# Optimization experiments

Hardware: AMD Instinct MI355X
Metric: run time of the kernel (lower is better)

## Reference

```python
import jax, jax.numpy as jnp
import numpy as np

N = 200_000   # nodes
E = 4_000_000 # edges
R = 4         # edge types
D = 64        # hidden_dim
V = 256       # opcode vocab
G = 64        # graphs in batch
C = 10        # classes


def setup_inputs() -> dict:
    key = jax.random.key(0)
    ks = jax.random.split(key, 24)
    inp = {
        "x_op": jax.random.randint(ks[0], (N,), 0, V, dtype=jnp.int32),
        "x_cat": jax.random.randint(ks[1], (N,), 0, 3, dtype=jnp.int32),
        "edge_index": jax.random.randint(ks[2], (2, E), 0, N, dtype=jnp.int32),
        "edge_type": jax.random.randint(ks[3], (E,), 0, R, dtype=jnp.int32),
        "batch": jnp.sort(jax.random.randint(ks[4], (N,), 0, G, dtype=jnp.int32)),
        "op_emb": jax.random.normal(ks[5], (V, D), jnp.float32) * 0.02,
        "cat_emb": jax.random.normal(ks[6], (3, D), jnp.float32) * 0.02,
    }
    for i in range(1, 4):
        inp[f"w{i}"] = jax.random.normal(ks[6 + 3 * i], (R, D, D), jnp.float32) * 0.02
        inp[f"r{i}"] = jax.random.normal(ks[7 + 3 * i], (D, D), jnp.float32) * 0.02
        inp[f"b{i}"] = jnp.zeros((D,), jnp.float32)
    inp["fc1_w"] = jax.random.normal(ks[20], (D, D), jnp.float32) * 0.02
    inp["fc1_b"] = jnp.zeros((D,), jnp.float32)
    inp["fc2_w"] = jax.random.normal(ks[21], (D, C), jnp.float32) * 0.02
    inp["fc2_b"] = jnp.zeros((C,), jnp.float32)
    return inp


def rgcn_layer(h, src, tgt, etype, w, root, bias):
    # PyG RGCNConv semantics: per-relation linear transform, per-relation
    # MEAN aggregation over incoming edges, summed over relations,
    # plus root transform and bias.
    n, d = h.shape
    r = w.shape[0]
    trans = jnp.einsum('nd,rde->rne', h, w)        # [R, N, d]
    msg = trans[etype, src]                         # [E, d] gather
    seg = tgt.astype(jnp.int32) * r + etype         # combined (node, relation) key
    s = jax.ops.segment_sum(msg, seg, num_segments=n * r)
    cnt = jax.ops.segment_sum(jnp.ones((msg.shape[0],), h.dtype), seg, num_segments=n * r)
    agg = (s / jnp.maximum(cnt, 1.0)[:, None]).reshape(n, r, d).sum(axis=1)
    return agg + h @ root + bias


def reference(x_op, x_cat, edge_index, edge_type, batch,
              op_emb, cat_emb,
              w1, r1, b1, w2, r2, b2, w3, r3, b3,
              fc1_w, fc1_b, fc2_w, fc2_b):
    src, tgt = edge_index[0], edge_index[1]
    h = op_emb[x_op] + cat_emb[x_cat]               # [N, D]
    h = jax.nn.relu(rgcn_layer(h, src, tgt, edge_type, w1, r1, b1))
    # dropout p=0.2 is identity in eval mode
    h = jax.nn.relu(rgcn_layer(h, src, tgt, edge_type, w2, r2, b2))
    h = rgcn_layer(h, src, tgt, edge_type, w3, r3, b3)
    # global mean pool over graphs
    sums = jax.ops.segment_sum(h, batch, num_segments=G)
    cnts = jax.ops.segment_sum(jnp.ones((h.shape[0],), h.dtype), batch, num_segments=G)
    pooled = sums / jnp.maximum(cnts, 1.0)[:, None]  # [G, D]
    h = jax.nn.relu(pooled @ fc1_w + fc1_b)
    out = h @ fc2_w + fc2_b
    return jax.nn.log_softmax(out, axis=1)
```

## Files before the change

### kernel.cpp

```cpp
#include <hip/hip_runtime.h>
#include <hip/hip_bf16.h>

#define N_NODES 200000
#define N_EDGES 4000000
#define R_REL   4
#define D_DIM   64
#define G_GRAPHS 64
#define C_CLS   10
#define NR      (N_NODES * R_REL)
#define POOL_BLOCKS 128

#define NCB   391
#define LCAP  64
#define CCAP  11264
#define EPB   8192

#define EMBED_BLOCKS 12500
#define BOUNDS_BLOCKS 782

#define MS    72

typedef __attribute__((ext_vector_type(8))) short short8v;
typedef __attribute__((ext_vector_type(4))) float f32x4;

__device__ __forceinline__ unsigned short to_bf16(float x) {
    __hip_bfloat16 b = __float2bfloat16(x);
    return *(unsigned short*)&b;
}

#define ACC8(u) \
    a0 += __uint_as_float((u).x << 16); \
    a1 += __uint_as_float((u).x & 0xFFFF0000u); \
    a2 += __uint_as_float((u).y << 16); \
    a3 += __uint_as_float((u).y & 0xFFFF0000u); \
    a4 += __uint_as_float((u).z << 16); \
    a5 += __uint_as_float((u).z & 0xFFFF0000u); \
    a6 += __uint_as_float((u).w << 16); \
    a7 += __uint_as_float((u).w & 0xFFFF0000u);


__global__ __launch_bounds__(512) void k_coarse(
    const int* __restrict__ src, const int* __restrict__ tgt,
    const int* __restrict__ et,
    int* __restrict__ gcur, unsigned int* __restrict__ coarse) {
    __shared__ unsigned int bins[NCB * LCAP];
    __shared__ int lcnt[NCB], lpos[NCB];

    const int tid = threadIdx.x;
    for (int i = tid; i < NCB; i += 512) lcnt[i] = 0;
    __syncthreads();

#pragma unroll
    for (int h = 0; h < 4; ++h) {
        int e4 = blockIdx.x * EPB + (h * 512 + tid) * 4;
        if (e4 < N_EDGES) {
            int4 s = *(const int4*)&src[e4];
            int4 t = *(const int4*)&tgt[e4];
            int4 r = *(const int4*)&et[e4];
#define PUT(ss, tt, rr) { \
                int key = (tt) * R_REL + (rr); \
                int b = key >> 11; \
                int p = atomicAdd(&lcnt[b], 1); \
                if (p < LCAP) bins[b * LCAP + p] = \
                    ((unsigned int)(key & 2047) << 18) | (unsigned int)(ss); \
            }
            PUT(s.x, t.x, r.x); PUT(s.y, t.y, r.y);
            PUT(s.z, t.z, r.z); PUT(s.w, t.w, r.w);
#undef PUT
        }
    }
    __syncthreads();

    for (int i = tid; i < NCB; i += 512) {
        int c = lcnt[i]; if (c > LCAP) c = LCAP;
        lcnt[i] = c;
        lpos[i] = atomicAdd(&gcur[i], c);
    }
    __syncthreads();

    for (int j = tid; j < NCB * LCAP; j += 512) {
        int b = j >> 6, l = j & 63;
        if (l < lcnt[b]) {
            int gp = lpos[b] + l;
            if (gp < CCAP) coarse[(size_t)b * CCAP + gp] = bins[j];
        }
    }
}


__global__ __launch_bounds__(1024) void k_fine(
    const int* __restrict__ gcur, const unsigned int* __restrict__ coarse,
    int* __restrict__ off, int* __restrict__ srcSorted) {
    __shared__ unsigned int ent[CCAP];
    __shared__ int hist[2048];
    __shared__ int pre[512];

    const int cb = blockIdx.x, tid = threadIdx.x;

    int v = 0;
    if (tid < 512) {
        v = (tid < NCB) ? gcur[tid] : 0;
        if (v > CCAP) v = CCAP;
        pre[tid] = v;
    }
    __syncthreads();
    for (int d = 1; d < 512; d <<= 1) {
        int t = 0;
        if (tid < 512 && tid >= d) t = pre[tid - d];
        __syncthreads();
        if (tid < 512) pre[tid] += t;
        __syncthreads();
    }
    const int gb = (cb > 0) ? pre[cb - 1] : 0;

    int cnt = gcur[cb]; if (cnt > CCAP) cnt = CCAP;
    const int key0 = cb << 11;
    const unsigned int* cp = coarse + (size_t)cb * CCAP;

    for (int i = tid; i < cnt; i += 1024) ent[i] = cp[i];
    hist[tid] = 0; hist[tid + 1024] = 0;
    __syncthreads();

    for (int i = tid; i < cnt; i += 1024) atomicAdd(&hist[ent[i] >> 18], 1);
    __syncthreads();

    int x0 = hist[tid], x1 = hist[tid + 1024];
    for (int d = 1; d < 2048; d <<= 1) {
        int v0 = (tid >= d) ? hist[tid - d] : 0;
        int v1 = hist[tid + 1024 - d];
        __syncthreads();
        hist[tid] += v0;
        hist[tid + 1024] += v1;
        __syncthreads();
    }
    int excl0 = hist[tid] - x0;
    int excl1 = hist[tid + 1024] - x1;
    __syncthreads();
    hist[tid] = excl0;
    hist[tid + 1024] = excl1;

    int key = key0 + tid;
    if (key < NR) off[key] = gb + excl0;
    key = key0 + tid + 1024;
    if (key < NR) off[key] = gb + excl1;
    if (cb == NCB - 1 && tid == 0) off[NR] = N_EDGES;
    __syncthreads();

    for (int i = tid; i < cnt; i += 1024) {
        unsigned int e = ent[i];
        int pos = atomicAdd(&hist[e >> 18], 1);
        srcSorted[gb + pos] = (int)(e & 0x3FFFFu);
    }
}


struct WPtrs { const float* p[15]; };

__global__ void k_misc(const int* __restrict__ xop, const int* __restrict__ xcat,
                       const float4* __restrict__ opemb, const float4* __restrict__ catemb,
                       ushort4* __restrict__ hb,
                       const int* __restrict__ batch, int* __restrict__ start,
                       WPtrs wp, unsigned short* __restrict__ wfrag) {
    int bid = blockIdx.x;
    if (bid < EMBED_BLOCKS) {
        int i = bid * 256 + threadIdx.x;
        if (i < N_NODES * 16) {
            int n = i >> 4, q = i & 15;
            float4 a = opemb[xop[n] * 16 + q];
            float4 b = catemb[xcat[n] * 16 + q];
            ushort4 ub;
            ub.x = to_bf16(a.x + b.x); ub.y = to_bf16(a.y + b.y);
            ub.z = to_bf16(a.z + b.z); ub.w = to_bf16(a.w + b.w);
            hb[i] = ub;
        }
    } else if (bid < EMBED_BLOCKS + BOUNDS_BLOCKS) {
        int i = (bid - EMBED_BLOCKS) * 256 + threadIdx.x;
        if (i >= N_NODES) return;
        int b = batch[i];
        if (i == 0) {
            for (int g = 0; g <= b; ++g) start[g] = 0;
        } else {
            int p = batch[i - 1];
            for (int g = p + 1; g <= b; ++g) start[g] = i;
        }
        if (i == N_NODES - 1) {
            for (int g = b + 1; g <= G_GRAPHS; ++g) start[g] = N_NODES;
        }
    } else {
        int m = bid - EMBED_BLOCKS - BOUNDS_BLOCKS;
        const float* W = wp.p[m];
        unsigned short* outp = wfrag + m * 4096;
        for (int f = threadIdx.x; f < 4096; f += 256) {
            int j = f & 7, lane = (f >> 3) & 63, c0t = (f >> 9) & 3, kk = f >> 11;
            int k  = kk * 32 + (lane >> 4) * 8 + j;
            int ch = c0t * 16 + (lane & 15);
            outp[f] = to_bf16(W[k * 64 + ch]);
        }
    }
}


template <int RELU>
__global__ __launch_bounds__(1024, 2) void k_layer(
    const unsigned short* __restrict__ hb_in,
    unsigned short* __restrict__ hb_out,
    const int* __restrict__ off, const int* __restrict__ srcSorted,
    const unsigned short* __restrict__ wfrag,
    const float* __restrict__ bias)
{
    __shared__ unsigned short m_lds[256 * MS];
    __shared__ unsigned short wf[5 * 4096];

    const int tid  = threadIdx.x;
    const int lane = tid & 63, wid = tid >> 6;
    const int g = lane >> 3, q = lane & 7;
    const int nbase = blockIdx.x * 64;

    for (int i = tid; i < 2560; i += 1024)
        ((uint4*)wf)[i] = ((const uint4*)wfrag)[i];

    const unsigned short* base = hb_in + q * 8;
#pragma unroll
    for (int p = 0; p < 2; ++p) {
        const int keyLocal = wid * 16 + p * 8 + g;
        const int key = nbase * R_REL + keyLocal;
        const int e0 = off[key];
        const int e1 = off[key + 1];

        float a0 = 0.f, a1 = 0.f, a2 = 0.f, a3 = 0.f,
              a4 = 0.f, a5 = 0.f, a6 = 0.f, a7 = 0.f;

        int e = e0;
        for (; e + 4 <= e1; e += 4) {
            int s0 = srcSorted[e];
            int s1 = srcSorted[e + 1];
            int s2 = srcSorted[e + 2];
            int s3 = srcSorted[e + 3];
            uint4 u0 = *(const uint4*)(base + (size_t)s0 * D_DIM);
            uint4 u1 = *(const uint4*)(base + (size_t)s1 * D_DIM);
            uint4 u2 = *(const uint4*)(base + (size_t)s2 * D_DIM);
            uint4 u3 = *(const uint4*)(base + (size_t)s3 * D_DIM);
            ACC8(u0); ACC8(u1); ACC8(u2); ACC8(u3);
        }
        for (; e < e1; ++e) {
            int s0 = srcSorted[e];
            uint4 u0 = *(const uint4*)(base + (size_t)s0 * D_DIM);
            ACC8(u0);
        }

        int deg = e1 - e0;
        const float iv = 1.0f / (float)(deg > 0 ? deg : 1);
        uint4 o;
        o.x = (unsigned int)to_bf16(a0 * iv) | ((unsigned int)to_bf16(a1 * iv) << 16);
        o.y = (unsigned int)to_bf16(a2 * iv) | ((unsigned int)to_bf16(a3 * iv) << 16);
        o.z = (unsigned int)to_bf16(a4 * iv) | ((unsigned int)to_bf16(a5 * iv) << 16);
        o.w = (unsigned int)to_bf16(a6 * iv) | ((unsigned int)to_bf16(a7 * iv) << 16);
        *(uint4*)(&m_lds[keyLocal * MS + q * 8]) = o;
    }
    __syncthreads();

    const int n0 = (wid >> 2) * 16;
    const int ct = wid & 3;
    const int arowL = n0 + (lane & 15);
    const int koff = (lane >> 4) * 8;

    f32x4 acc = {0.f, 0.f, 0.f, 0.f};

#pragma unroll
    for (int r = 0; r < 5; ++r) {
        uint4 a0u, a1u;
        if (r < 4) {
            const unsigned short* ap = &m_lds[(arowL * R_REL + r) * MS];
            a0u = *(const uint4*)(ap + koff);
            a1u = *(const uint4*)(ap + 32 + koff);
        } else {
            const unsigned short* ap = hb_in + (size_t)(nbase + arowL) * D_DIM;
            a0u = *(const uint4*)(ap + koff);
            a1u = *(const uint4*)(ap + 32 + koff);
        }
        const unsigned short* bbase = wf + r * 4096 + ct * 512 + lane * 8;
        uint4 b0u = *(const uint4*)bbase;
        uint4 b1u = *(const uint4*)(bbase + 2048);
        acc = __builtin_amdgcn_mfma_f32_16x16x32_bf16(
            __builtin_bit_cast(short8v, a0u), __builtin_bit_cast(short8v, b0u), acc, 0, 0, 0);
        acc = __builtin_amdgcn_mfma_f32_16x16x32_bf16(
            __builtin_bit_cast(short8v, a1u), __builtin_bit_cast(short8v, b1u), acc, 0, 0, 0);
    }

    float bv = bias[ct * 16 + (lane & 15)];
#pragma unroll
    for (int i = 0; i < 4; ++i) {
        float v = acc[i] + bv;
        if (RELU) v = fmaxf(v, 0.f);
        int n = nbase + n0 + (lane >> 4) * 4 + i;
        hb_out[(size_t)n * D_DIM + ct * 16 + (lane & 15)] = to_bf16(v);
    }
}


__global__ __launch_bounds__(1024) void k_pool(const unsigned short* __restrict__ hb,
                                               const int* __restrict__ batch,
                                               float* __restrict__ partial) {
    __shared__ float bin[G_GRAPHS * D_DIM];
    int tid = threadIdx.x, lane = tid & 63, wid = tid >> 6;
    for (int i = tid; i < G_GRAPHS * D_DIM; i += 1024) bin[i] = 0.f;
    __syncthreads();
    const int per = (N_NODES + POOL_BLOCKS - 1) / POOL_BLOCKS;
    int n0 = blockIdx.x * per;
    int n1 = n0 + per; if (n1 > N_NODES) n1 = N_NODES;
    int cntw = n1 - n0;
    int sub = (cntw + 15) >> 4;
    int w0 = n0 + wid * sub;
    int w1 = w0 + sub; if (w1 > n1) w1 = n1;

    float acc = 0.f;
    int cur = -1;
    for (int n = w0; n < w1; ++n) {
        int b = __builtin_amdgcn_readfirstlane(batch[n]);
        unsigned int u = hb[(size_t)n * D_DIM + lane];
        float v = __uint_as_float(u << 16);
        if (b != cur) {
            if (cur >= 0) atomicAdd(&bin[cur * D_DIM + lane], acc);
            cur = b;
            acc = v;
        } else {
            acc += v;
        }
    }
    if (cur >= 0) atomicAdd(&bin[cur * D_DIM + lane], acc);
    __syncthreads();
    for (int i = tid; i < G_GRAPHS * D_DIM; i += 1024)
        partial[blockIdx.x * (G_GRAPHS * D_DIM) + i] = bin[i];
}

__global__ void k_pool_reduce(const float* __restrict__ partial,
                              float* __restrict__ pooled) {
    int i = blockIdx.x * blockDim.x + threadIdx.x;
    if (i < G_GRAPHS * D_DIM) {
        float s = 0.f;
        for (int b = 0; b < POOL_BLOCKS; ++b) s += partial[b * (G_GRAPHS * D_DIM) + i];
        pooled[i] = s;
    }
}


__global__ void k_head(const float* __restrict__ pooled, const int* __restrict__ start,
                       const float* __restrict__ fc1w, const float* __restrict__ fc1b,
                       const float* __restrict__ fc2w, const float* __restrict__ fc2b,
                       float* __restrict__ out) {
    __shared__ float p[G_GRAPHS][D_DIM];
    __shared__ float hf[G_GRAPHS][D_DIM];
    __shared__ float sc[G_GRAPHS][C_CLS];
    int t = threadIdx.x;

    for (int i = t; i < G_GRAPHS * D_DIM; i += 1024) {
        int g = i >> 6;
        int c = start[g + 1] - start[g];
        p[g][i & 63] = pooled[i] / (float)(c > 0 ? c : 1);
    }
    __syncthreads();

    for (int i = t; i < G_GRAPHS * D_DIM; i += 1024) {
        int g = i >> 6, o = i & 63;
        float a = fc1b[o];
#pragma unroll
        for (int d = 0; d < D_DIM; ++d) a = fmaf(p[g][d], fc1w[d * D_DIM + o], a);
        hf[g][o] = fmaxf(a, 0.f);
    }
    __syncthreads();

    if (t < G_GRAPHS * C_CLS) {
        int g = t / C_CLS, c = t % C_CLS;
        float a = fc2b[c];
#pragma unroll
        for (int d = 0; d < D_DIM; ++d) a = fmaf(hf[g][d], fc2w[d * C_CLS + c], a);
        sc[g][c] = a;
    }
    __syncthreads();

    if (t < G_GRAPHS) {
        float m = -1e30f;
#pragma unroll
        for (int c = 0; c < C_CLS; ++c) m = fmaxf(m, sc[t][c]);
        float s = 0.f;
#pragma unroll
        for (int c = 0; c < C_CLS; ++c) s += expf(sc[t][c] - m);
        float lse = m + logf(s);
#pragma unroll
        for (int c = 0; c < C_CLS; ++c) out[t * C_CLS + c] = sc[t][c] - lse;
    }
}


extern "C" void kernel_launch(void* const* d_in, const int* in_sizes, int n_in,
                              void* d_out, int out_size, void* d_ws, size_t ws_size,
                              hipStream_t stream) {
    const int*   x_op    = (const int*)d_in[0];
    const int*   x_cat   = (const int*)d_in[1];
    const int*   eidx    = (const int*)d_in[2];
    const int*   src     = eidx;
    const int*   tgt     = eidx + N_EDGES;
    const int*   etype   = (const int*)d_in[3];
    const int*   batch   = (const int*)d_in[4];
    const float* op_emb  = (const float*)d_in[5];
    const float* cat_emb = (const float*)d_in[6];
    const float* w1 = (const float*)d_in[7];
    const float* r1 = (const float*)d_in[8];
    const float* b1 = (const float*)d_in[9];
    const float* w2 = (const float*)d_in[10];
    const float* r2 = (const float*)d_in[11];
    const float* b2 = (const float*)d_in[12];
    const float* w3 = (const float*)d_in[13];
    const float* r3 = (const float*)d_in[14];
    const float* b3 = (const float*)d_in[15];
    const float* fc1w = (const float*)d_in[16];
    const float* fc1b = (const float*)d_in[17];
    const float* fc2w = (const float*)d_in[18];
    const float* fc2b = (const float*)d_in[19];
    float* out = (float*)d_out;

    char* ws = (char*)d_ws;
    size_t o = 0;
    auto alloc = [&](size_t bytes) -> void* {
        o = (o + 255) & ~(size_t)255;
        void* p = ws + o;
        o += bytes;
        return p;
    };

    int*   off        = (int*)alloc((size_t)(NR + 1) * 4);
    int*   srcSorted  = (int*)alloc((size_t)N_EDGES * 4);
    unsigned short* hb0   = (unsigned short*)alloc((size_t)N_NODES * D_DIM * 2);
    unsigned short* hb1   = (unsigned short*)alloc((size_t)N_NODES * D_DIM * 2);
    unsigned int*   coarse = (unsigned int*)alloc((size_t)NCB * CCAP * 4);
    unsigned short* wfrag = (unsigned short*)alloc((size_t)15 * 4096 * 2);
    float* partial    = (float*)alloc((size_t)POOL_BLOCKS * G_GRAPHS * D_DIM * 4);
    float* pooled     = (float*)alloc((size_t)G_GRAPHS * D_DIM * 4);
    int*   startg     = (int*)alloc((size_t)(G_GRAPHS + 1) * 4);
    int*   gcur       = (int*)alloc((size_t)NCB * 4);

    hipMemsetAsync(gcur, 0, (size_t)NCB * 4, stream);

    k_coarse<<<(N_EDGES + EPB - 1) / EPB, 512, 0, stream>>>(src, tgt, etype, gcur, coarse);
    k_fine<<<NCB, 1024, 0, stream>>>(gcur, coarse, off, srcSorted);

    WPtrs wp;
    wp.p[0] = w1;          wp.p[1] = w1 + 4096;  wp.p[2] = w1 + 8192;  wp.p[3] = w1 + 12288;
    wp.p[4] = r1;
    wp.p[5] = w2;          wp.p[6] = w2 + 4096;  wp.p[7] = w2 + 8192;  wp.p[8] = w2 + 12288;
    wp.p[9] = r2;
    wp.p[10] = w3;         wp.p[11] = w3 + 4096; wp.p[12] = w3 + 8192; wp.p[13] = w3 + 12288;
    wp.p[14] = r3;
    k_misc<<<EMBED_BLOCKS + BOUNDS_BLOCKS + 15, 256, 0, stream>>>(
        x_op, x_cat, (const float4*)op_emb, (const float4*)cat_emb, (ushort4*)hb0,
        batch, startg, wp, wfrag);

    const int layerBlocks = N_NODES / 64;

    k_layer<1><<<layerBlocks, 1024, 0, stream>>>(hb0, hb1, off, srcSorted, wfrag, b1);
    k_layer<1><<<layerBlocks, 1024, 0, stream>>>(hb1, hb0, off, srcSorted, wfrag + 5 * 4096, b2);
    k_layer<0><<<layerBlocks, 1024, 0, stream>>>(hb0, hb1, off, srcSorted, wfrag + 10 * 4096, b3);

    k_pool<<<POOL_BLOCKS, 1024, 0, stream>>>(hb1, batch, partial);
    k_pool_reduce<<<(G_GRAPHS * D_DIM + 255) / 256, 256, 0, stream>>>(partial, pooled);
    k_head<<<1, 1024, 0, stream>>>(pooled, startg, fc1w, fc1b, fc2w, fc2b, out);
}
```

Baseline: 426.7 us.

## Gather neighbor features from a scaled FP8 copy and halve layer block size

```diff
diff --git a/kernel.cpp b/kernel.cpp
--- a/kernel.cpp
+++ b/kernel.cpp
@@ -1,5 +1,6 @@
 #include <hip/hip_runtime.h>
 #include <hip/hip_bf16.h>
+#include <hip/hip_fp8.h>
 
 #define N_NODES 200000
 #define N_EDGES 4000000
@@ -19,6 +20,8 @@
 #define BOUNDS_BLOCKS 782
 
 #define MS    72
+#define H8SCALE 64.0f
+#define H8INV   (1.0f / 64.0f)
 
 typedef __attribute__((ext_vector_type(8))) short short8v;
 typedef __attribute__((ext_vector_type(4))) float f32x4;
@@ -27,16 +30,25 @@
     __hip_bfloat16 b = __float2bfloat16(x);
     return *(unsigned short*)&b;
 }
-
-#define ACC8(u) \
-    a0 += __uint_as_float((u).x << 16); \
-    a1 += __uint_as_float((u).x & 0xFFFF0000u); \
-    a2 += __uint_as_float((u).y << 16); \
-    a3 += __uint_as_float((u).y & 0xFFFF0000u); \
-    a4 += __uint_as_float((u).z << 16); \
-    a5 += __uint_as_float((u).z & 0xFFFF0000u); \
-    a6 += __uint_as_float((u).w << 16); \
-    a7 += __uint_as_float((u).w & 0xFFFF0000u);
+__device__ __forceinline__ unsigned char to_fp8(float x) {
+    __hip_fp8_e4m3 v(x);
+    return *(unsigned char*)&v;
+}
+__device__ __forceinline__ float from_fp8(unsigned int b) {
+    __hip_fp8_e4m3 v;
+    v.__x = (__hip_fp8_storage_t)b;
+    return (float)v;
+}
+
+#define ACC8F8(u) \
+    a0 += from_fp8((u).x & 255);         \
+    a1 += from_fp8(((u).x >> 8) & 255);  \
+    a2 += from_fp8(((u).x >> 16) & 255); \
+    a3 += from_fp8((u).x >> 24);         \
+    a4 += from_fp8((u).y & 255);         \
+    a5 += from_fp8(((u).y >> 8) & 255);  \
+    a6 += from_fp8(((u).y >> 16) & 255); \
+    a7 += from_fp8((u).y >> 24);
 
 
 __global__ __launch_bounds__(512) void k_coarse(
@@ -158,7 +170,7 @@
 
 __global__ void k_misc(const int* __restrict__ xop, const int* __restrict__ xcat,
                        const float4* __restrict__ opemb, const float4* __restrict__ catemb,
-                       ushort4* __restrict__ hb,
+                       ushort4* __restrict__ hb, uchar4* __restrict__ hb8,
                        const int* __restrict__ batch, int* __restrict__ start,
                        WPtrs wp, unsigned short* __restrict__ wfrag) {
     int bid = blockIdx.x;
@@ -168,10 +180,15 @@
             int n = i >> 4, q = i & 15;
             float4 a = opemb[xop[n] * 16 + q];
             float4 b = catemb[xcat[n] * 16 + q];
+            float4 r = make_float4(a.x + b.x, a.y + b.y, a.z + b.z, a.w + b.w);
             ushort4 ub;
-            ub.x = to_bf16(a.x + b.x); ub.y = to_bf16(a.y + b.y);
-            ub.z = to_bf16(a.z + b.z); ub.w = to_bf16(a.w + b.w);
+            ub.x = to_bf16(r.x); ub.y = to_bf16(r.y);
+            ub.z = to_bf16(r.z); ub.w = to_bf16(r.w);
             hb[i] = ub;
+            uchar4 u8;
+            u8.x = to_fp8(r.x * H8SCALE); u8.y = to_fp8(r.y * H8SCALE);
+            u8.z = to_fp8(r.z * H8SCALE); u8.w = to_fp8(r.w * H8SCALE);
+            hb8[i] = u8;
         }
     } else if (bid < EMBED_BLOCKS + BOUNDS_BLOCKS) {
         int i = (bid - EMBED_BLOCKS) * 256 + threadIdx.x;
@@ -201,28 +218,26 @@
 
 
 template <int RELU>
-__global__ __launch_bounds__(1024, 2) void k_layer(
+__global__ __launch_bounds__(512) void k_layer(
     const unsigned short* __restrict__ hb_in,
+    const unsigned char*  __restrict__ hb8_in,
     unsigned short* __restrict__ hb_out,
+    unsigned char*  __restrict__ hb8_out,
     const int* __restrict__ off, const int* __restrict__ srcSorted,
     const unsigned short* __restrict__ wfrag,
     const float* __restrict__ bias)
 {
     __shared__ unsigned short m_lds[256 * MS];
-    __shared__ unsigned short wf[5 * 4096];
 
     const int tid  = threadIdx.x;
     const int lane = tid & 63, wid = tid >> 6;
     const int g = lane >> 3, q = lane & 7;
     const int nbase = blockIdx.x * 64;
 
-    for (int i = tid; i < 2560; i += 1024)
-        ((uint4*)wf)[i] = ((const uint4*)wfrag)[i];
-
-    const unsigned short* base = hb_in + q * 8;
-#pragma unroll
-    for (int p = 0; p < 2; ++p) {
-        const int keyLocal = wid * 16 + p * 8 + g;
+    const unsigned char* base8 = hb8_in + q * 8;
+#pragma unroll
+    for (int p = 0; p < 4; ++p) {
+        const int keyLocal = wid * 32 + p * 8 + g;
         const int key = nbase * R_REL + keyLocal;
         const int e0 = off[key];
         const int e1 = off[key + 1];
@@ -236,20 +251,20 @@
             int s1 = srcSorted[e + 1];
             int s2 = srcSorted[e + 2];
             int s3 = srcSorted[e + 3];
-            uint4 u0 = *(const uint4*)(base + (size_t)s0 * D_DIM);
-            uint4 u1 = *(const uint4*)(base + (size_t)s1 * D_DIM);
-            uint4 u2 = *(const uint4*)(base + (size_t)s2 * D_DIM);
-            uint4 u3 = *(const uint4*)(base + (size_t)s3 * D_DIM);
-            ACC8(u0); ACC8(u1); ACC8(u2); ACC8(u3);
+            uint2 u0 = *(const uint2*)(base8 + (size_t)s0 * D_DIM);
+            uint2 u1 = *(const uint2*)(base8 + (size_t)s1 * D_DIM);
+            uint2 u2 = *(const uint2*)(base8 + (size_t)s2 * D_DIM);
+            uint2 u3 = *(const uint2*)(base8 + (size_t)s3 * D_DIM);
+            ACC8F8(u0); ACC8F8(u1); ACC8F8(u2); ACC8F8(u3);
         }
         for (; e < e1; ++e) {
             int s0 = srcSorted[e];
-            uint4 u0 = *(const uint4*)(base + (size_t)s0 * D_DIM);
-            ACC8(u0);
+            uint2 u0 = *(const uint2*)(base8 + (size_t)s0 * D_DIM);
+            ACC8F8(u0);
         }
 
         int deg = e1 - e0;
-        const float iv = 1.0f / (float)(deg > 0 ? deg : 1);
+        const float iv = H8INV / (float)(deg > 0 ? deg : 1);
         uint4 o;
         o.x = (unsigned int)to_bf16(a0 * iv) | ((unsigned int)to_bf16(a1 * iv) << 16);
         o.y = (unsigned int)to_bf16(a2 * iv) | ((unsigned int)to_bf16(a3 * iv) << 16);
@@ -259,41 +274,48 @@
     }
     __syncthreads();
 
-    const int n0 = (wid >> 2) * 16;
     const int ct = wid & 3;
-    const int arowL = n0 + (lane & 15);
+    const int ntBase = wid >> 2;
     const int koff = (lane >> 4) * 8;
-
-    f32x4 acc = {0.f, 0.f, 0.f, 0.f};
-
-#pragma unroll
-    for (int r = 0; r < 5; ++r) {
-        uint4 a0u, a1u;
-        if (r < 4) {
-            const unsigned short* ap = &m_lds[(arowL * R_REL + r) * MS];
-            a0u = *(const uint4*)(ap + koff);
-            a1u = *(const uint4*)(ap + 32 + koff);
-        } else {
-            const unsigned short* ap = hb_in + (size_t)(nbase + arowL) * D_DIM;
-            a0u = *(const uint4*)(ap + koff);
-            a1u = *(const uint4*)(ap + 32 + koff);
-        }
-        const unsigned short* bbase = wf + r * 4096 + ct * 512 + lane * 8;
-        uint4 b0u = *(const uint4*)bbase;
-        uint4 b1u = *(const uint4*)(bbase + 2048);
-        acc = __builtin_amdgcn_mfma_f32_16x16x32_bf16(
-            __builtin_bit_cast(short8v, a0u), __builtin_bit_cast(short8v, b0u), acc, 0, 0, 0);
-        acc = __builtin_amdgcn_mfma_f32_16x16x32_bf16(
-            __builtin_bit_cast(short8v, a1u), __builtin_bit_cast(short8v, b1u), acc, 0, 0, 0);
-    }
-
-    float bv = bias[ct * 16 + (lane & 15)];
-#pragma unroll
-    for (int i = 0; i < 4; ++i) {
-        float v = acc[i] + bv;
-        if (RELU) v = fmaxf(v, 0.f);
-        int n = nbase + n0 + (lane >> 4) * 4 + i;
-        hb_out[(size_t)n * D_DIM + ct * 16 + (lane & 15)] = to_bf16(v);
+    const float bv = bias[ct * 16 + (lane & 15)];
+
+#pragma unroll
+    for (int tt = 0; tt < 2; ++tt) {
+        const int n0 = (ntBase + tt * 2) * 16;
+        const int arowL = n0 + (lane & 15);
+
+        f32x4 acc = {0.f, 0.f, 0.f, 0.f};
+
+#pragma unroll
+        for (int r = 0; r < 5; ++r) {
+            uint4 a0u, a1u;
+            if (r < 4) {
+                const unsigned short* ap = &m_lds[(arowL * R_REL + r) * MS];
+                a0u = *(const uint4*)(ap + koff);
+                a1u = *(const uint4*)(ap + 32 + koff);
+            } else {
+                const unsigned short* ap = hb_in + (size_t)(nbase + arowL) * D_DIM;
+                a0u = *(const uint4*)(ap + koff);
+                a1u = *(const uint4*)(ap + 32 + koff);
+            }
+            const unsigned short* bbase = wfrag + r * 4096 + ct * 512 + lane * 8;
+            uint4 b0u = *(const uint4*)bbase;
+            uint4 b1u = *(const uint4*)(bbase + 2048);
+            acc = __builtin_amdgcn_mfma_f32_16x16x32_bf16(
+                __builtin_bit_cast(short8v, a0u), __builtin_bit_cast(short8v, b0u), acc, 0, 0, 0);
+            acc = __builtin_amdgcn_mfma_f32_16x16x32_bf16(
+                __builtin_bit_cast(short8v, a1u), __builtin_bit_cast(short8v, b1u), acc, 0, 0, 0);
+        }
+
+#pragma unroll
+        for (int i = 0; i < 4; ++i) {
+            float v = acc[i] + bv;
+            if (RELU) v = fmaxf(v, 0.f);
+            int n = nbase + n0 + (lane >> 4) * 4 + i;
+            hb_out[(size_t)n * D_DIM + ct * 16 + (lane & 15)] = to_bf16(v);
+            if (RELU)
+                hb8_out[(size_t)n * D_DIM + ct * 16 + (lane & 15)] = to_fp8(v * H8SCALE);
+        }
     }
 }
 
@@ -432,6 +454,8 @@
     int*   srcSorted  = (int*)alloc((size_t)N_EDGES * 4);
     unsigned short* hb0   = (unsigned short*)alloc((size_t)N_NODES * D_DIM * 2);
     unsigned short* hb1   = (unsigned short*)alloc((size_t)N_NODES * D_DIM * 2);
+    unsigned char*  hb8_0 = (unsigned char*)alloc((size_t)N_NODES * D_DIM);
+    unsigned char*  hb8_1 = (unsigned char*)alloc((size_t)N_NODES * D_DIM);
     unsigned int*   coarse = (unsigned int*)alloc((size_t)NCB * CCAP * 4);
     unsigned short* wfrag = (unsigned short*)alloc((size_t)15 * 4096 * 2);
     float* partial    = (float*)alloc((size_t)POOL_BLOCKS * G_GRAPHS * D_DIM * 4);
@@ -452,14 +476,17 @@
     wp.p[10] = w3;         wp.p[11] = w3 + 4096; wp.p[12] = w3 + 8192; wp.p[13] = w3 + 12288;
     wp.p[14] = r3;
     k_misc<<<EMBED_BLOCKS + BOUNDS_BLOCKS + 15, 256, 0, stream>>>(
-        x_op, x_cat, (const float4*)op_emb, (const float4*)cat_emb, (ushort4*)hb0,
-        batch, startg, wp, wfrag);
+        x_op, x_cat, (const float4*)op_emb, (const float4*)cat_emb,
+        (ushort4*)hb0, (uchar4*)hb8_0, batch, startg, wp, wfrag);
 
     const int layerBlocks = N_NODES / 64;
 
-    k_layer<1><<<layerBlocks, 1024, 0, stream>>>(hb0, hb1, off, srcSorted, wfrag, b1);
-    k_layer<1><<<layerBlocks, 1024, 0, stream>>>(hb1, hb0, off, srcSorted, wfrag + 5 * 4096, b2);
-    k_layer<0><<<layerBlocks, 1024, 0, stream>>>(hb0, hb1, off, srcSorted, wfrag + 10 * 4096, b3);
+    k_layer<1><<<layerBlocks, 512, 0, stream>>>(
+        hb0, hb8_0, hb1, hb8_1, off, srcSorted, wfrag, b1);
+    k_layer<1><<<layerBlocks, 512, 0, stream>>>(
+        hb1, hb8_1, hb0, hb8_0, off, srcSorted, wfrag + 5 * 4096, b2);
+    k_layer<0><<<layerBlocks, 512, 0, stream>>>(
+        hb0, hb8_0, hb1, hb8_1, off, srcSorted, wfrag + 10 * 4096, b3);
 
     k_pool<<<POOL_BLOCKS, 1024, 0, stream>>>(hb1, batch, partial);
     k_pool_reduce<<<(G_GRAPHS * D_DIM + 255) / 256, 256, 0, stream>>>(partial, pooled);
```

New measurement: 428.3 us. No clear change (+0.4%).

## Halve layer block size, unroll gather by eight, read weights from global

Applied to the files above, without the earlier changes.

```diff
diff --git a/kernel.cpp b/kernel.cpp
--- a/kernel.cpp
+++ b/kernel.cpp
@@ -201,7 +201,7 @@
 
 
 template <int RELU>
-__global__ __launch_bounds__(1024, 2) void k_layer(
+__global__ __launch_bounds__(512) void k_layer(
     const unsigned short* __restrict__ hb_in,
     unsigned short* __restrict__ hb_out,
     const int* __restrict__ off, const int* __restrict__ srcSorted,
@@ -209,43 +209,41 @@
     const float* __restrict__ bias)
 {
     __shared__ unsigned short m_lds[256 * MS];
-    __shared__ unsigned short wf[5 * 4096];
 
     const int tid  = threadIdx.x;
     const int lane = tid & 63, wid = tid >> 6;
     const int g = lane >> 3, q = lane & 7;
     const int nbase = blockIdx.x * 64;
 
-    for (int i = tid; i < 2560; i += 1024)
-        ((uint4*)wf)[i] = ((const uint4*)wfrag)[i];
-
     const unsigned short* base = hb_in + q * 8;
 #pragma unroll
-    for (int p = 0; p < 2; ++p) {
-        const int keyLocal = wid * 16 + p * 8 + g;
+    for (int p = 0; p < 4; ++p) {
+        const int keyLocal = wid * 32 + p * 8 + g;
         const int key = nbase * R_REL + keyLocal;
         const int e0 = off[key];
         const int e1 = off[key + 1];
+        const int last = e1 - 1;
 
         float a0 = 0.f, a1 = 0.f, a2 = 0.f, a3 = 0.f,
               a4 = 0.f, a5 = 0.f, a6 = 0.f, a7 = 0.f;
 
-        int e = e0;
-        for (; e + 4 <= e1; e += 4) {
-            int s0 = srcSorted[e];
-            int s1 = srcSorted[e + 1];
-            int s2 = srcSorted[e + 2];
-            int s3 = srcSorted[e + 3];
-            uint4 u0 = *(const uint4*)(base + (size_t)s0 * D_DIM);
-            uint4 u1 = *(const uint4*)(base + (size_t)s1 * D_DIM);
-            uint4 u2 = *(const uint4*)(base + (size_t)s2 * D_DIM);
-            uint4 u3 = *(const uint4*)(base + (size_t)s3 * D_DIM);
-            ACC8(u0); ACC8(u1); ACC8(u2); ACC8(u3);
-        }
-        for (; e < e1; ++e) {
-            int s0 = srcSorted[e];
-            uint4 u0 = *(const uint4*)(base + (size_t)s0 * D_DIM);
-            ACC8(u0);
+        for (int e = e0; e < e1; e += 8) {
+            int s[8];
+#pragma unroll
+            for (int k = 0; k < 8; ++k) {
+                int ee = e + k;
+                ee = (ee > last) ? last : ee;
+                s[k] = srcSorted[ee];
+            }
+            uint4 u[8];
+#pragma unroll
+            for (int k = 0; k < 8; ++k)
+                u[k] = *(const uint4*)(base + (size_t)s[k] * D_DIM);
+            const int rem = e1 - e;
+#pragma unroll
+            for (int k = 0; k < 8; ++k) {
+                if (k < rem) { ACC8(u[k]); }
+            }
         }
 
         int deg = e1 - e0;
@@ -259,41 +257,46 @@
     }
     __syncthreads();
 
-    const int n0 = (wid >> 2) * 16;
     const int ct = wid & 3;
-    const int arowL = n0 + (lane & 15);
+    const int ntBase = wid >> 2;
     const int koff = (lane >> 4) * 8;
-
-    f32x4 acc = {0.f, 0.f, 0.f, 0.f};
-
-#pragma unroll
-    for (int r = 0; r < 5; ++r) {
-        uint4 a0u, a1u;
-        if (r < 4) {
-            const unsigned short* ap = &m_lds[(arowL * R_REL + r) * MS];
-            a0u = *(const uint4*)(ap + koff);
-            a1u = *(const uint4*)(ap + 32 + koff);
-        } else {
-            const unsigned short* ap = hb_in + (size_t)(nbase + arowL) * D_DIM;
-            a0u = *(const uint4*)(ap + koff);
-            a1u = *(const uint4*)(ap + 32 + koff);
-        }
-        const unsigned short* bbase = wf + r * 4096 + ct * 512 + lane * 8;
-        uint4 b0u = *(const uint4*)bbase;
-        uint4 b1u = *(const uint4*)(bbase + 2048);
-        acc = __builtin_amdgcn_mfma_f32_16x16x32_bf16(
-            __builtin_bit_cast(short8v, a0u), __builtin_bit_cast(short8v, b0u), acc, 0, 0, 0);
-        acc = __builtin_amdgcn_mfma_f32_16x16x32_bf16(
-            __builtin_bit_cast(short8v, a1u), __builtin_bit_cast(short8v, b1u), acc, 0, 0, 0);
-    }
-
-    float bv = bias[ct * 16 + (lane & 15)];
-#pragma unroll
-    for (int i = 0; i < 4; ++i) {
-        float v = acc[i] + bv;
-        if (RELU) v = fmaxf(v, 0.f);
-        int n = nbase + n0 + (lane >> 4) * 4 + i;
-        hb_out[(size_t)n * D_DIM + ct * 16 + (lane & 15)] = to_bf16(v);
+    const float bv = bias[ct * 16 + (lane & 15)];
+
+#pragma unroll
+    for (int tt = 0; tt < 2; ++tt) {
+        const int n0 = (ntBase + tt * 2) * 16;
+        const int arowL = n0 + (lane & 15);
+
+        f32x4 acc = {0.f, 0.f, 0.f, 0.f};
+
+#pragma unroll
+        for (int r = 0; r < 5; ++r) {
+            uint4 a0u, a1u;
+            if (r < 4) {
+                const unsigned short* ap = &m_lds[(arowL * R_REL + r) * MS];
+                a0u = *(const uint4*)(ap + koff);
+                a1u = *(const uint4*)(ap + 32 + koff);
+            } else {
+                const unsigned short* ap = hb_in + (size_t)(nbase + arowL) * D_DIM;
+                a0u = *(const uint4*)(ap + koff);
+                a1u = *(const uint4*)(ap + 32 + koff);
+            }
+            const unsigned short* bbase = wfrag + r * 4096 + ct * 512 + lane * 8;
+            uint4 b0u = *(const uint4*)bbase;
+            uint4 b1u = *(const uint4*)(bbase + 2048);
+            acc = __builtin_amdgcn_mfma_f32_16x16x32_bf16(
+                __builtin_bit_cast(short8v, a0u), __builtin_bit_cast(short8v, b0u), acc, 0, 0, 0);
+            acc = __builtin_amdgcn_mfma_f32_16x16x32_bf16(
+                __builtin_bit_cast(short8v, a1u), __builtin_bit_cast(short8v, b1u), acc, 0, 0, 0);
+        }
+
+#pragma unroll
+        for (int i = 0; i < 4; ++i) {
+            float v = acc[i] + bv;
+            if (RELU) v = fmaxf(v, 0.f);
+            int n = nbase + n0 + (lane >> 4) * 4 + i;
+            hb_out[(size_t)n * D_DIM + ct * 16 + (lane & 15)] = to_bf16(v);
+        }
     }
 }
 
@@ -457,9 +460,9 @@
 
     const int layerBlocks = N_NODES / 64;
 
-    k_layer<1><<<layerBlocks, 1024, 0, stream>>>(hb0, hb1, off, srcSorted, wfrag, b1);
-    k_layer<1><<<layerBlocks, 1024, 0, stream>>>(hb1, hb0, off, srcSorted, wfrag + 5 * 4096, b2);
-    k_layer<0><<<layerBlocks, 1024, 0, stream>>>(hb0, hb1, off, srcSorted, wfrag + 10 * 4096, b3);
+    k_layer<1><<<layerBlocks, 512, 0, stream>>>(hb0, hb1, off, srcSorted, wfrag, b1);
+    k_layer<1><<<layerBlocks, 512, 0, stream>>>(hb1, hb0, off, srcSorted, wfrag + 5 * 4096, b2);
+    k_layer<0><<<layerBlocks, 512, 0, stream>>>(hb0, hb1, off, srcSorted, wfrag + 10 * 4096, b3);
 
     k_pool<<<POOL_BLOCKS, 1024, 0, stream>>>(hb1, batch, partial);
     k_pool_reduce<<<(G_GRAPHS * D_DIM + 255) / 256, 256, 0, stream>>>(partial, pooled);
```

Result: faster. 407.2 us (-4.6%).
